# Performance work log

Measured on AMD Instinct MI355X. Metric: run time of the kernel, lower is better.

The kernel has to match this reference:

```python
import jax, jax.numpy as jnp
from jax import lax
import numpy as np

T, C_IN, H, W = 32, 64, 128, 128
C_OUT, KH, KW = 128, 5, 5
H_OUT, W_OUT = H - KH + 1, W - KW + 1  # 124, 124
K_WINNERS = 256
LR_PLUS, LR_MINUS = 0.004, -0.003
LOWER, UPPER = 0.0, 1.0


def setup_inputs() -> dict:
    key = jax.random.key(0)
    k1, k2, k3, k4, k5, k6 = jax.random.split(key, 6)
    input_spikes = (jax.random.uniform(k1, (T, C_IN, H, W)) < 0.1).astype(jnp.float32)
    output_spikes = (jax.random.uniform(k2, (T, C_OUT, H_OUT, W_OUT)) < 0.05).astype(jnp.float32)
    weight = jax.random.uniform(k3, (C_OUT, C_IN, KH, KW), dtype=jnp.float32)
    f = jax.random.randint(k4, (K_WINNERS,), 0, C_OUT, dtype=jnp.int32)
    r = jax.random.randint(k5, (K_WINNERS,), 0, H_OUT, dtype=jnp.int32)
    c = jax.random.randint(k6, (K_WINNERS,), 0, W_OUT, dtype=jnp.int32)
    winners = jnp.stack([f, r, c], axis=1)  # [K, 3]
    return {"input_spikes": input_spikes, "output_spikes": output_spikes,
            "weight": weight, "winners": winners}


def reference(input_spikes, output_spikes, weight, winners):
    # latencies: sum spikes over time
    in_lat = jnp.sum(input_spikes, axis=0)    # [C_in, H, W]
    out_lat = jnp.sum(output_spikes, axis=0)  # [C_out, H_out, W_out]

    # gather per-winner input patches [K, C_in, kh, kw]
    def patch(rc):
        return lax.dynamic_slice(in_lat, (0, rc[0], rc[1]), (C_IN, KH, KW))
    patches = jax.vmap(patch)(winners[:, 1:])

    out_vals = out_lat[winners[:, 0], winners[:, 1], winners[:, 2]]  # [K]
    pair = patches >= out_vals[:, None, None, None]                  # [K, C_in, kh, kw]
    lr_vals = jnp.where(pair, LR_PLUS, LR_MINUS).astype(weight.dtype)

    # sequential scatter: later winners overwrite earlier ones (matches torch loop)
    def step(lr, inp):
        idx, val = inp
        return lr.at[idx].set(val), None
    lr, _ = lax.scan(step, jnp.zeros_like(weight), (winners[:, 0], lr_vals))

    stab = (weight - LOWER) * (UPPER - weight)  # use_stabilizer=True
    new_w = weight + lr * stab
    return jnp.clip(new_w, LOWER, UPPER)
```

## Files before the change

kernel.cpp:

```cpp
#include <hip/hip_runtime.h>

#define T 32
#define C_IN 64
#define H 128
#define W 128
#define C_OUT 128
#define KH 5
#define KW 5
#define H_OUT 124
#define W_OUT 124
#define K_WINNERS 256
#define LR_PLUS 0.004f
#define LR_MINUS -0.003f


__global__ void winner_prep(const float* __restrict__ out_spikes,
                            const int* __restrict__ winners,
                            int* __restrict__ win_idx,
                            float* __restrict__ out_val) {
    __shared__ int s_win[C_OUT];
    const int tid = threadIdx.x;
    if (tid < C_OUT) s_win[tid] = -1;
    __syncthreads();
    if (tid < K_WINNERS) {
        int f = winners[tid * 3];
        atomicMax(&s_win[f], tid);
    }
    __syncthreads();
    if (tid < C_OUT) {
        int k = s_win[tid];
        win_idx[tid] = k;
        float v = 0.0f;
        if (k >= 0) {
            int r = winners[k * 3 + 1];
            int c = winners[k * 3 + 2];
            const float* p = out_spikes + (size_t)tid * (H_OUT * W_OUT)
                                        + (size_t)r * W_OUT + c;
            #pragma unroll
            for (int t = 0; t < T; ++t)
                v += p[(size_t)t * (C_OUT * H_OUT * W_OUT)];
        }
        out_val[tid] = v;
    }
}

__global__ void stdp_update(const float* __restrict__ in_spikes,
                            const int* __restrict__ winners,
                            const float* __restrict__ weight,
                            const int* __restrict__ win_idx,
                            const float* __restrict__ out_val,
                            float* __restrict__ out) {
    const int idx = blockIdx.x * blockDim.x + threadIdx.x;
    const int f   = idx / (C_IN * KH * KW);
    const int rem = idx % (C_IN * KH * KW);
    const int ci  = rem / (KH * KW);
    const int p   = rem % (KH * KW);
    const int kh  = p / KW;
    const int kw  = p % KW;

    float w = weight[idx];
    int k = win_idx[f];
    float res;
    if (k < 0) {
        res = w;
    } else {
        int r = winners[k * 3 + 1] + kh;
        int c = winners[k * 3 + 2] + kw;
        const float* ptr = in_spikes + (size_t)ci * (H * W) + (size_t)r * W + c;
        float sum = 0.0f;
        #pragma unroll
        for (int t = 0; t < T; ++t)
            sum += ptr[(size_t)t * (C_IN * H * W)];
        float lr = (sum >= out_val[f]) ? LR_PLUS : LR_MINUS;
        res = w + lr * w * (1.0f - w);
    }
    res = fminf(fmaxf(res, 0.0f), 1.0f);
    out[idx] = res;
}

extern "C" void kernel_launch(void* const* d_in, const int* in_sizes, int n_in,
                              void* d_out, int out_size, void* d_ws, size_t ws_size,
                              hipStream_t stream) {
    const float* in_spikes  = (const float*)d_in[0];
    const float* out_spikes = (const float*)d_in[1];
    const float* weight     = (const float*)d_in[2];
    const int*   winners    = (const int*)d_in[3];
    float* out = (float*)d_out;

    int*   win_idx = (int*)d_ws;
    float* out_val = (float*)((char*)d_ws + C_OUT * sizeof(int));

    winner_prep<<<1, 256, 0, stream>>>(out_spikes, winners, win_idx, out_val);

    const int total = C_OUT * C_IN * KH * KW;
    stdp_update<<<total / 256, 256, 0, stream>>>(in_spikes, winners, weight,
                                                 win_idx, out_val, out);
}
```

Measured before the change: 375.1 us.

## Fuse winner preparation into the STDP update kernel with per-filter blocks

Merges the single-block winner_prep kernel into the main update kernel. Each block now handles one output filter (5 blocks of 320 threads per filter), finds the last winner for that filter with a shared-memory atomicMax, and gathers the 32 output-spike values in parallel rather than serially in one thread. This removes a kernel launch and the serialized single-block prep stage. In exchange, every block redundantly scans the winners array and has extra barriers.

After: 365.2 us. 2.6% less time.

```diff
diff --git a/kernel.cpp b/kernel.cpp
--- a/kernel.cpp
+++ b/kernel.cpp
@@ -13,69 +13,68 @@
 #define LR_PLUS 0.004f
 #define LR_MINUS -0.003f
 
+#define BLOCKS_PER_F 5
+#define BLOCK 320
 
-__global__ void winner_prep(const float* __restrict__ out_spikes,
-                            const int* __restrict__ winners,
-                            int* __restrict__ win_idx,
-                            float* __restrict__ out_val) {
-    __shared__ int s_win[C_OUT];
+__global__ __launch_bounds__(BLOCK) void stdp_fused(
+        const float* __restrict__ in_spikes,
+        const float* __restrict__ out_spikes,
+        const float* __restrict__ weight,
+        const int* __restrict__ winners,
+        float* __restrict__ out) {
+    __shared__ int s_k;
+    __shared__ float s_part[T];
+    __shared__ float s_outval;
+
+    const int f = blockIdx.x / BLOCKS_PER_F;
     const int tid = threadIdx.x;
-    if (tid < C_OUT) s_win[tid] = -1;
+
+    if (tid == 0) s_k = -1;
     __syncthreads();
-    if (tid < K_WINNERS) {
-        int f = winners[tid * 3];
-        atomicMax(&s_win[f], tid);
+    if (tid < K_WINNERS && winners[tid * 3] == f)
+        atomicMax(&s_k, tid);
+    __syncthreads();
+    const int k = s_k;
+
+    int r0 = 0, c0 = 0;
+    if (k >= 0) {
+        r0 = winners[k * 3 + 1];
+        c0 = winners[k * 3 + 2];
+        if (tid < T) {
+            s_part[tid] = out_spikes[(size_t)tid * (C_OUT * H_OUT * W_OUT)
+                                     + (size_t)f * (H_OUT * W_OUT)
+                                     + (size_t)r0 * W_OUT + c0];
+        }
     }
     __syncthreads();
-    if (tid < C_OUT) {
-        int k = s_win[tid];
-        win_idx[tid] = k;
+    if (k >= 0 && tid == 0) {
         float v = 0.0f;
-        if (k >= 0) {
-            int r = winners[k * 3 + 1];
-            int c = winners[k * 3 + 2];
-            const float* p = out_spikes + (size_t)tid * (H_OUT * W_OUT)
-                                        + (size_t)r * W_OUT + c;
-            #pragma unroll
-            for (int t = 0; t < T; ++t)
-                v += p[(size_t)t * (C_OUT * H_OUT * W_OUT)];
-        }
-        out_val[tid] = v;
+        #pragma unroll
+        for (int t = 0; t < T; ++t) v += s_part[t];
+        s_outval = v;
     }
-}
+    __syncthreads();
 
-__global__ void stdp_update(const float* __restrict__ in_spikes,
-                            const int* __restrict__ winners,
-                            const float* __restrict__ weight,
-                            const int* __restrict__ win_idx,
-                            const float* __restrict__ out_val,
-                            float* __restrict__ out) {
-    const int idx = blockIdx.x * blockDim.x + threadIdx.x;
-    const int f   = idx / (C_IN * KH * KW);
-    const int rem = idx % (C_IN * KH * KW);
-    const int ci  = rem / (KH * KW);
-    const int p   = rem % (KH * KW);
-    const int kh  = p / KW;
-    const int kw  = p % KW;
-
+    const int rem = (blockIdx.x % BLOCKS_PER_F) * BLOCK + tid;
+    const int idx = f * (C_IN * KH * KW) + rem;
     float w = weight[idx];
-    int k = win_idx[f];
     float res;
     if (k < 0) {
         res = w;
     } else {
-        int r = winners[k * 3 + 1] + kh;
-        int c = winners[k * 3 + 2] + kw;
+        const int ci = rem / (KH * KW);
+        const int p  = rem % (KH * KW);
+        const int r  = r0 + p / KW;
+        const int c  = c0 + p % KW;
         const float* ptr = in_spikes + (size_t)ci * (H * W) + (size_t)r * W + c;
         float sum = 0.0f;
         #pragma unroll
         for (int t = 0; t < T; ++t)
             sum += ptr[(size_t)t * (C_IN * H * W)];
-        float lr = (sum >= out_val[f]) ? LR_PLUS : LR_MINUS;
+        float lr = (sum >= s_outval) ? LR_PLUS : LR_MINUS;
         res = w + lr * w * (1.0f - w);
     }
-    res = fminf(fmaxf(res, 0.0f), 1.0f);
-    out[idx] = res;
+    out[idx] = fminf(fmaxf(res, 0.0f), 1.0f);
 }
 
 extern "C" void kernel_launch(void* const* d_in, const int* in_sizes, int n_in,
@@ -87,12 +86,6 @@
     const int*   winners    = (const int*)d_in[3];
     float* out = (float*)d_out;
 
-    int*   win_idx = (int*)d_ws;
-    float* out_val = (float*)((char*)d_ws + C_OUT * sizeof(int));
-
-    winner_prep<<<1, 256, 0, stream>>>(out_spikes, winners, win_idx, out_val);
-
-    const int total = C_OUT * C_IN * KH * KW;
-    stdp_update<<<total / 256, 256, 0, stream>>>(in_spikes, winners, weight,
-                                                 win_idx, out_val, out);
+    stdp_fused<<<C_OUT * BLOCKS_PER_F, BLOCK, 0, stream>>>(
+        in_spikes, out_spikes, weight, winners, out);
 }
```
